# Optimization experiments

Hardware: AMD Instinct MI355X
Metric: run time of the kernel (lower is better)

## Reference

```python
import jax, jax.numpy as jnp
import numpy as np

B, S, D, E = 32, 16, 64, 768  # batch, max summary segments, max doc splits, embed dim
EPS = 1e-12


def _l2norm(x):
    # tf.nn.l2_normalize: x * rsqrt(max(sum(x^2), eps))
    return x * jax.lax.rsqrt(jnp.maximum(jnp.sum(x * x, axis=-1, keepdims=True), EPS))


def setup_inputs() -> dict:
    key = jax.random.key(0)
    ks = jax.random.split(key, 12)
    nd = jax.random.randint(ks[0], (B,), 1, D + 1)
    ns = jax.random.randint(ks[1], (B,), 1, S + 1)
    doc = jax.random.normal(ks[2], (B, D, E), jnp.float32)
    seg = jax.random.normal(ks[3], (B, S, E), jnp.float32)
    # emulate RaggedTensor.to_tensor(): zero padding beyond ragged lengths
    doc = doc * (jnp.arange(D)[None, :, None] < nd[:, None, None])
    seg = seg * (jnp.arange(S)[None, :, None] < ns[:, None, None])
    tis = jax.random.uniform(ks[4], (B, S), jnp.float32)
    tis = jnp.where(jnp.arange(S)[None, :] < ns[:, None], tis, 1.0)
    tagg = jax.random.uniform(ks[5], (B,), jnp.float32)
    s1, s2, s3 = 1.0 / np.sqrt(2 * E), 1.0 / np.sqrt(E), 1.0 / np.sqrt(E // 2)
    W1 = jax.random.normal(ks[6], (2 * E, E), jnp.float32) * s1
    W2 = jax.random.normal(ks[7], (E, E // 2), jnp.float32) * s2
    W3 = jax.random.normal(ks[8], (E // 2, 1), jnp.float32) * s3
    return {
        'document_splits_embedding': doc,
        'summary_sentences_embedding': seg,
        'num_document_splits': nd,
        'num_summary_segments': ns,
        'target_agg_score': tagg,
        'target_instance_score': tis,
        'W1': W1, 'b1': jnp.zeros((E,), jnp.float32),
        'W2': W2, 'b2': jnp.zeros((E // 2,), jnp.float32),
        'W3': W3, 'b3': jnp.zeros((1,), jnp.float32),
    }


def reference(document_splits_embedding, summary_sentences_embedding,
              num_document_splits, num_summary_segments,
              target_agg_score, target_instance_score,
              W1, b1, W2, b2, W3, b3):
    doc, seg = document_splits_embedding, summary_sentences_embedding
    nd, ns = num_document_splits, num_summary_segments
    b, d, e = doc.shape
    s = seg.shape[1]
    nsf = ns.astype(jnp.float32)

    # target_instance_score padded with 1.0 beyond ragged length (done in setup; pass through)
    tis = target_instance_score

    # ---- pairwise MLP over all (segment, doc_split) pairs ----
    pair = jnp.concatenate([
        jnp.broadcast_to(doc[:, None, :, :], (b, s, d, e)),
        jnp.broadcast_to(seg[:, :, None, :], (b, s, d, e)),
    ], axis=-1)                                             # [B,S,D,2E]
    h = jax.nn.gelu(pair @ W1 + b1, approximate=False)      # [B,S,D,E]
    h = jax.nn.gelu(h @ W2 + b2, approximate=False)         # [B,S,D,E/2]
    mlp_out = jax.nn.sigmoid(h @ W3 + b3)[..., 0]           # [B,S,D]

    doc_mask = (jnp.arange(d)[None, :] < nd[:, None]).astype(jnp.float32)  # [B,D]
    scored = doc_mask[:, None, :] * mlp_out                # mask invalid doc splits
    pred0 = jnp.max(scored, axis=2)                         # [B,S]
    seg_scale = jnp.where(ns > 10, 1.0, 100.0)[:, None]     # faithful to mask+(1-mask)*100
    pred = seg_scale * pred0                                # [B,S]

    # ---- cosine similarity prior (keras CosineSimilarity = -cos) ----
    dn = _l2norm(doc)                                       # [B,D,E]
    sn = _l2norm(seg)                                       # [B,S,E]
    cos = jnp.einsum('bse,bde->bsd', sn, dn)                # [B,S,D]
    sim = doc_mask[:, None, :] * (1.0 + (-cos)) / 2.0
    doc_cos = jnp.max(sim, axis=2)                          # [B,S]
    seg_mask = (jnp.arange(s)[None, :] < ns[:, None]).astype(jnp.float32)
    diff = jnp.abs(doc_cos - pred) * seg_mask
    cos_prior = jnp.mean(jnp.sum(diff, axis=1) / nsf)

    # ---- correlation prior: Pearson correlation over the 768 'sample' axis ----
    c = seg - jnp.mean(seg, axis=-1, keepdims=True)
    z = c * jax.lax.rsqrt(jnp.maximum(jnp.sum(c * c, axis=-1, keepdims=True), EPS))
    R = (1.0 + jnp.einsum('bse,bte->bst', z, z)) / 2.0      # [B,S,S]
    p = pred
    t1 = (1.0 - p)[:, :, None] * (1.0 - p)[:, None, :]
    t2 = p[:, :, None] * p[:, None, :]
    pair_mask = seg_mask[:, :, None] * seg_mask[:, None, :]
    term = jnp.abs(t1 - R) * jnp.abs(t2 - R) * pair_mask
    corr_prior = jnp.mean(jnp.sum(term, axis=(1, 2)) / nsf)

    return (target_agg_score, tis, pred, ns, cos_prior, corr_prior)
```

## Files before the change

### kernel.cpp

```cpp
#include <hip/hip_runtime.h>
#include <hip/hip_bf16.h>
#include <math.h>

#define EPSF 1e-12f

typedef short bf16x8 __attribute__((ext_vector_type(8)));
typedef float f32x4  __attribute__((ext_vector_type(4)));

__device__ __forceinline__ float gelu_fast(float x) {
    float x2 = x * x;
    float z = -2.3021184f * x * fmaf(0.044715f, x2, 1.0f);
    float u = __builtin_amdgcn_exp2f(z);
    return x * __builtin_amdgcn_rcpf(1.0f + u);
}
__device__ __forceinline__ float sigmoid_fast(float x) {
    float u = __builtin_amdgcn_exp2f(-1.44269504f * x);
    return __builtin_amdgcn_rcpf(1.0f + u);
}
__device__ __forceinline__ float bf2f(unsigned short u) {
    return __uint_as_float(((unsigned int)u) << 16);
}
__device__ __forceinline__ unsigned short f2bf(float f) {
    unsigned int u = __float_as_uint(f);
    u += 0x7FFFu + ((u >> 16) & 1u);
    return (unsigned short)(u >> 16);
}

__global__ __launch_bounds__(256) void k_prep(
    const float* __restrict__ doc, const float* __restrict__ seg,
    const float* __restrict__ W1, const float* __restrict__ W2,
    const float* __restrict__ tagg, const float* __restrict__ tis,
    const int* __restrict__ ns,
    float* __restrict__ dscale, float* __restrict__ sscale,
    float* __restrict__ smean, float* __restrict__ cscale,
    unsigned short* __restrict__ docB, unsigned short* __restrict__ segB,
    unsigned short* __restrict__ W1T, unsigned short* __restrict__ W2T,
    float* __restrict__ out)
{
    __shared__ float sT[64][65];
    int blk = blockIdx.x;
    int t = threadIdx.x;
    if (blk == 1000) {
        if (t < 32) out[t] = tagg[t];
        out[32 + t] = tis[t];
        out[32 + 256 + t] = tis[256 + t];
        if (t < 32) out[1056 + t] = (float)ns[t];
        return;
    }
    if (blk < 640) {
        int row = blk * 4 + (t >> 6);
        int lane = t & 63;
        const float* src = (row < 2048) ? (doc + (size_t)row * 768)
                                        : (seg + (size_t)(row - 2048) * 768);
        unsigned short* dst = (row < 2048) ? (docB + (size_t)row * 768)
                                           : (segB + (size_t)(row - 2048) * 768);
        float ss = 0.f, sm = 0.f;
        float4 v0 = *(const float4*)(src + lane * 4);
        float4 v1 = *(const float4*)(src + lane * 4 + 256);
        float4 v2 = *(const float4*)(src + lane * 4 + 512);
        ss += v0.x * v0.x + v0.y * v0.y + v0.z * v0.z + v0.w * v0.w;
        ss += v1.x * v1.x + v1.y * v1.y + v1.z * v1.z + v1.w * v1.w;
        ss += v2.x * v2.x + v2.y * v2.y + v2.z * v2.z + v2.w * v2.w;
        sm += v0.x + v0.y + v0.z + v0.w;
        sm += v1.x + v1.y + v1.z + v1.w;
        sm += v2.x + v2.y + v2.z + v2.w;
        {
            ushort4 o;
            o.x = f2bf(v0.x); o.y = f2bf(v0.y); o.z = f2bf(v0.z); o.w = f2bf(v0.w);
            *(ushort4*)(dst + lane * 4) = o;
            o.x = f2bf(v1.x); o.y = f2bf(v1.y); o.z = f2bf(v1.z); o.w = f2bf(v1.w);
            *(ushort4*)(dst + lane * 4 + 256) = o;
            o.x = f2bf(v2.x); o.y = f2bf(v2.y); o.z = f2bf(v2.z); o.w = f2bf(v2.w);
            *(ushort4*)(dst + lane * 4 + 512) = o;
        }
        #pragma unroll
        for (int off = 32; off > 0; off >>= 1) {
            ss += __shfl_down(ss, off);
            sm += __shfl_down(sm, off);
        }
        if (lane == 0) {
            if (row < 2048) {
                dscale[row] = rsqrtf(fmaxf(ss, EPSF));
            } else {
                int r = row - 2048;
                sscale[r] = rsqrtf(fmaxf(ss, EPSF));
                float mean = sm * (1.0f / 768.0f);
                smean[r] = mean;
                cscale[r] = rsqrtf(fmaxf(ss - sm * mean, EPSF));
            }
        }
        return;
    }
    int tt = blk - 640;
    const float* in; unsigned short* out2; int R, C, bx, by;
    if (tt < 288) { in = W1; out2 = W1T; R = 1536; C = 768; bx = tt % 12; by = tt / 12; }
    else { tt -= 288; in = W2; out2 = W2T; R = 768; C = 384; bx = tt % 6; by = tt / 6; }
    int c0 = bx * 64, r0 = by * 64;
    int tr = t >> 2, tc4 = (t & 3) * 16;
    #pragma unroll
    for (int i = 0; i < 4; ++i) {
        float4 v = *(const float4*)(in + (size_t)(r0 + tr) * C + c0 + tc4 + i * 4);
        sT[tr][tc4 + i * 4 + 0] = v.x; sT[tr][tc4 + i * 4 + 1] = v.y;
        sT[tr][tc4 + i * 4 + 2] = v.z; sT[tr][tc4 + i * 4 + 3] = v.w;
    }
    __syncthreads();
    union { uint4 v; unsigned short u[8]; } o0, o1;
    #pragma unroll
    for (int i = 0; i < 8; ++i) o0.u[i] = f2bf(sT[tc4 + i][tr]);
    #pragma unroll
    for (int i = 0; i < 8; ++i) o1.u[i] = f2bf(sT[tc4 + 8 + i][tr]);
    *(uint4*)(out2 + (size_t)(c0 + tr) * R + r0 + tc4) = o0.v;
    *(uint4*)(out2 + (size_t)(c0 + tr) * R + r0 + tc4 + 8) = o1.v;
}

__global__ __launch_bounds__(256) void k_l1(
    const unsigned short* __restrict__ docB, const unsigned short* __restrict__ segB,
    const unsigned short* __restrict__ W1T_bf, const float* __restrict__ b1,
    unsigned short* __restrict__ XdocB, unsigned short* __restrict__ XsegB)
{
    int mb = blockIdx.x;
    int n0 = blockIdx.y * 128;
    int t = threadIdx.x, w = t >> 6, l = t & 63;
    int lm = l & 15, kh = l >> 4;
    bool isdoc = (mb < 32);
    int m0 = isdoc ? mb * 64 : (mb - 32) * 64;
    const unsigned short* A = isdoc ? docB : segB;
    int koff = isdoc ? 0 : 768;
    unsigned short* C = isdoc ? XdocB : XsegB;

    const unsigned short* gA = A + (size_t)(m0 + lm) * 768 + kh * 8;
    const unsigned short* gB = W1T_bf + (size_t)(n0 + w * 32 + lm) * 1536 + koff + kh * 8;

    f32x4 acc[4][2];
    #pragma unroll
    for (int mt = 0; mt < 4; ++mt)
        #pragma unroll
        for (int nt = 0; nt < 2; ++nt) acc[mt][nt] = (f32x4){0.f, 0.f, 0.f, 0.f};

    bf16x8 a0A[4], a1A[4], b0A[2], b1A[2];
    bf16x8 a0B[4], a1B[4], b0B[2], b1B[2];
    #pragma unroll
    for (int mt = 0; mt < 4; ++mt) {
        a0A[mt] = *(const bf16x8*)(gA + (size_t)mt * 16 * 768);
        a1A[mt] = *(const bf16x8*)(gA + (size_t)mt * 16 * 768 + 32);
    }
    #pragma unroll
    for (int nt = 0; nt < 2; ++nt) {
        b0A[nt] = *(const bf16x8*)(gB + (size_t)nt * 16 * 1536);
        b1A[nt] = *(const bf16x8*)(gB + (size_t)nt * 16 * 1536 + 32);
    }

    #define L1_BODY(KT, A0, A1, B0, B1, NA0, NA1, NB0, NB1)                     \
    {                                                                           \
        if ((KT) < 11) {                                                        \
            int ko = ((KT) + 1) * 64;                                           \
            _Pragma("unroll")                                                   \
            for (int mt = 0; mt < 4; ++mt) {                                    \
                NA0[mt] = *(const bf16x8*)(gA + (size_t)mt * 16 * 768 + ko);    \
                NA1[mt] = *(const bf16x8*)(gA + (size_t)mt * 16 * 768 + ko + 32); \
            }                                                                   \
            _Pragma("unroll")                                                   \
            for (int nt = 0; nt < 2; ++nt) {                                    \
                NB0[nt] = *(const bf16x8*)(gB + (size_t)nt * 16 * 1536 + ko);   \
                NB1[nt] = *(const bf16x8*)(gB + (size_t)nt * 16 * 1536 + ko + 32); \
            }                                                                   \
        }                                                                       \
        _Pragma("unroll")                                                       \
        for (int mt = 0; mt < 4; ++mt)                                          \
            _Pragma("unroll")                                                   \
            for (int nt = 0; nt < 2; ++nt)                                      \
                acc[mt][nt] = __builtin_amdgcn_mfma_f32_16x16x32_bf16(          \
                    A0[mt], B0[nt], acc[mt][nt], 0, 0, 0);                      \
        _Pragma("unroll")                                                       \
        for (int mt = 0; mt < 4; ++mt)                                          \
            _Pragma("unroll")                                                   \
            for (int nt = 0; nt < 2; ++nt)                                      \
                acc[mt][nt] = __builtin_amdgcn_mfma_f32_16x16x32_bf16(          \
                    A1[mt], B1[nt], acc[mt][nt], 0, 0, 0);                      \
    }

    for (int kt2 = 0; kt2 < 12; kt2 += 2) {
        L1_BODY(kt2,     a0A, a1A, b0A, b1A, a0B, a1B, b0B, b1B);
        L1_BODY(kt2 + 1, a0B, a1B, b0B, b1B, a0A, a1A, b0A, b1A);
    }
    #undef L1_BODY

    #pragma unroll
    for (int nt = 0; nt < 2; ++nt) {
        int n = n0 + w * 32 + nt * 16 + lm;
        float bv = isdoc ? 0.f : b1[n];
        #pragma unroll
        for (int mt = 0; mt < 4; ++mt)
            #pragma unroll
            for (int j = 0; j < 4; ++j) {
                int row = m0 + mt * 16 + kh * 4 + j;
                C[(size_t)row * 768 + n] = f2bf(acc[mt][nt][j] + bv);
            }
    }
}

__global__ __launch_bounds__(256, 2) void k_fused_mfma(
    const unsigned short* __restrict__ XdocB, const unsigned short* __restrict__ XsegB,
    const unsigned short* __restrict__ W2T_bf,
    const float* __restrict__ b2, const float* __restrict__ W3, const float* __restrict__ b3,
    const int* __restrict__ nd, const int* __restrict__ ns,
    const unsigned short* __restrict__ docB, const unsigned short* __restrict__ segB,
    const float* __restrict__ seg,
    const float* __restrict__ dscale, const float* __restrict__ sscale,
    const float* __restrict__ smean, const float* __restrict__ cscale,
    float* __restrict__ out_pred, float* __restrict__ predv,
    float* __restrict__ dcws, float* __restrict__ Rws)
{
    __shared__ union {
        struct {
            unsigned short sA0[64 * 64];
            unsigned short sA1[64 * 64];
            float sXseg[768];
            float sRed[64][4];
        } p;
        struct { float sRedC[16][4]; } c;
        struct { unsigned short zb[16][776]; } r;
    } U;

    int blk = blockIdx.x;
    int t = threadIdx.x, w = t >> 6, l = t & 63;
    int lm = l & 15, kh = l >> 4;

    if (blk >= 512) {
        if (blk < 544) {
            int b = blk - 512;
            const unsigned short* gS = segB + (size_t)(b * 16 + lm) * 768 + kh * 8;
            const unsigned short* gD = docB + (size_t)(b * 64 + w * 16 + lm) * 768 + kh * 8;
            f32x4 acc = (f32x4){0.f, 0.f, 0.f, 0.f};
            for (int kt = 0; kt < 24; ++kt) {
                bf16x8 a = *(const bf16x8*)(gS + kt * 32);
                bf16x8 bb = *(const bf16x8*)(gD + kt * 32);
                acc = __builtin_amdgcn_mfma_f32_16x16x32_bf16(a, bb, acc, 0, 0, 0);
            }
            int ndb = nd[b];
            int d = w * 16 + lm;
            float dsc = dscale[b * 64 + d];
            #pragma unroll
            for (int j = 0; j < 4; ++j) {
                int s = kh * 4 + j;
                float cosv = acc[j] * sscale[b * 16 + s] * dsc;
                float sim = (d < ndb) ? (1.0f - cosv) * 0.5f : 0.f;
                sim = fmaxf(sim, __shfl_xor(sim, 1));
                sim = fmaxf(sim, __shfl_xor(sim, 2));
                sim = fmaxf(sim, __shfl_xor(sim, 4));
                sim = fmaxf(sim, __shfl_xor(sim, 8));
                if (lm == 0) U.c.sRedC[s][w] = sim;
            }
            __syncthreads();
            if (t < 16) {
                float dc = fmaxf(fmaxf(U.c.sRedC[t][0], U.c.sRedC[t][1]),
                                 fmaxf(U.c.sRedC[t][2], U.c.sRedC[t][3]));
                dcws[b * 16 + t] = dc;
            }
        } else {
            int b = blk - 544;
            for (int i = t; i < 16 * 768; i += 256) {
                int s = i / 768; int e = i - s * 768;
                U.r.zb[s][e] = f2bf((seg[((size_t)b * 16 + s) * 768 + e]
                                     - smean[b * 16 + s]) * cscale[b * 16 + s]);
            }
            __syncthreads();
            if (w == 0) {
                f32x4 acc = (f32x4){0.f, 0.f, 0.f, 0.f};
                #pragma unroll
                for (int kt = 0; kt < 24; ++kt) {
                    bf16x8 z = *(const bf16x8*)&U.r.zb[lm][kt * 32 + kh * 8];
                    acc = __builtin_amdgcn_mfma_f32_16x16x32_bf16(z, z, acc, 0, 0, 0);
                }
                #pragma unroll
                for (int j = 0; j < 4; ++j) {
                    int row = kh * 4 + j;
                    Rws[b * 256 + row * 16 + lm] = 0.5f * (1.0f + acc[j]);
                }
            }
        }
        return;
    }

    int bs = ((blk & 7) << 6) | (blk >> 3);
    int b = bs >> 4;
    int sw2 = (lm & 7) << 4;

    for (int i = t; i < 768; i += 256) U.p.sXseg[i] = bf2f(XsegB[(size_t)bs * 768 + i]);

    const int ndb = nd[b];
    const float segscale = (ns[b] > 10) ? 1.0f : 100.0f;
    const float b3v = b3[0];

    f32x4 acc[4][6];
    #pragma unroll
    for (int mt = 0; mt < 4; ++mt)
        #pragma unroll
        for (int nt = 0; nt < 6; ++nt) acc[mt][nt] = (f32x4){0.f, 0.f, 0.f, 0.f};

    int ar = t >> 2, ak = (t & 3) * 16;
    int asw = (ar & 7) << 4;
    const char* gXd = (const char*)XdocB + (size_t)(b * 64 + ar) * 1536;
    const unsigned short* gW2w = W2T_bf + (size_t)(w * 96 + lm) * 768 + kh * 8;

    union u128 { uint4 v; unsigned short u[8]; };

    bf16x8 bbA[6], bbB[6];
    #pragma unroll
    for (int nt = 0; nt < 6; ++nt)
        bbA[nt] = *(const bf16x8*)(gW2w + (size_t)nt * 16 * 768);

    {
        u128 xc0, xc1;
        xc0.v = *(const uint4*)(gXd + ak * 2);
        xc1.v = *(const uint4*)(gXd + ak * 2 + 16);
        __syncthreads();
        u128 o0, o1;
        #pragma unroll
        for (int i = 0; i < 8; ++i)
            o0.u[i] = f2bf(gelu_fast(bf2f(xc0.u[i]) + U.p.sXseg[ak + i]));
        #pragma unroll
        for (int i = 0; i < 8; ++i)
            o1.u[i] = f2bf(gelu_fast(bf2f(xc1.u[i]) + U.p.sXseg[ak + 8 + i]));
        *(uint4*)((char*)U.p.sA0 + ar * 128 + ((ak * 2) ^ asw)) = o0.v;
        *(uint4*)((char*)U.p.sA0 + ar * 128 + ((ak * 2 + 16) ^ asw)) = o1.v;
    }

    #pragma unroll
    for (int kt = 0; kt < 12; ++kt) {
        unsigned short* cbuf = (kt & 1) ? U.p.sA1 : U.p.sA0;
        unsigned short* nbuf = (kt & 1) ? U.p.sA0 : U.p.sA1;
        __syncthreads();
        u128 xn0, xn1;
        if (kt < 11) {
            xn0.v = *(const uint4*)(gXd + (kt + 1) * 128 + ak * 2);
            xn1.v = *(const uint4*)(gXd + (kt + 1) * 128 + ak * 2 + 16);
        }
        {
            #pragma unroll
            for (int nt = 0; nt < 6; ++nt)
                bbB[nt] = *(const bf16x8*)(gW2w + (size_t)nt * 16 * 768 + kt * 64 + 32);
            int kb = (kh * 16) ^ sw2;
            bf16x8 a[4];
            #pragma unroll
            for (int mt = 0; mt < 4; ++mt)
                a[mt] = *(const bf16x8*)((const char*)cbuf + (mt * 16 + lm) * 128 + kb);
            __builtin_amdgcn_s_setprio(1);
            #pragma unroll
            for (int mt = 0; mt < 4; ++mt)
                #pragma unroll
                for (int nt = 0; nt < 6; ++nt)
                    acc[mt][nt] = __builtin_amdgcn_mfma_f32_16x16x32_bf16(
                        a[mt], bbA[nt], acc[mt][nt], 0, 0, 0);
            __builtin_amdgcn_s_setprio(0);
        }
        {
            if (kt < 11) {
                #pragma unroll
                for (int nt = 0; nt < 6; ++nt)
                    bbA[nt] = *(const bf16x8*)(gW2w + (size_t)nt * 16 * 768 + (kt + 1) * 64);
            }
            int kb = (64 + kh * 16) ^ sw2;
            bf16x8 a[4];
            #pragma unroll
            for (int mt = 0; mt < 4; ++mt)
                a[mt] = *(const bf16x8*)((const char*)cbuf + (mt * 16 + lm) * 128 + kb);
            __builtin_amdgcn_s_setprio(1);
            #pragma unroll
            for (int mt = 0; mt < 4; ++mt)
                #pragma unroll
                for (int nt = 0; nt < 6; ++nt)
                    acc[mt][nt] = __builtin_amdgcn_mfma_f32_16x16x32_bf16(
                        a[mt], bbB[nt], acc[mt][nt], 0, 0, 0);
            __builtin_amdgcn_s_setprio(0);
        }
        if (kt < 11) {
            u128 o0, o1;
            #pragma unroll
            for (int i = 0; i < 8; ++i)
                o0.u[i] = f2bf(gelu_fast(bf2f(xn0.u[i]) + U.p.sXseg[(kt + 1) * 64 + ak + i]));
            #pragma unroll
            for (int i = 0; i < 8; ++i)
                o1.u[i] = f2bf(gelu_fast(bf2f(xn1.u[i]) + U.p.sXseg[(kt + 1) * 64 + ak + 8 + i]));
            *(uint4*)((char*)nbuf + ar * 128 + ((ak * 2) ^ asw)) = o0.v;
            *(uint4*)((char*)nbuf + ar * 128 + ((ak * 2 + 16) ^ asw)) = o1.v;
        }
    }

    float b2v[6], w3v[6];
    #pragma unroll
    for (int nt = 0; nt < 6; ++nt) {
        int n = w * 96 + nt * 16 + lm;
        b2v[nt] = b2[n]; w3v[nt] = W3[n];
    }
    #pragma unroll
    for (int mt = 0; mt < 4; ++mt) {
        #pragma unroll
        for (int j = 0; j < 4; ++j) {
            float s = 0.f;
            #pragma unroll
            for (int nt = 0; nt < 6; ++nt)
                s += gelu_fast(acc[mt][nt][j] + b2v[nt]) * w3v[nt];
            s += __shfl_xor(s, 1); s += __shfl_xor(s, 2);
            s += __shfl_xor(s, 4); s += __shfl_xor(s, 8);
            if (lm == 0) U.p.sRed[mt * 16 + kh * 4 + j][w] = s;
        }
    }
    __syncthreads();
    if (w == 0) {
        float h3 = U.p.sRed[l][0] + U.p.sRed[l][1] + U.p.sRed[l][2] + U.p.sRed[l][3] + b3v;
        float sig = sigmoid_fast(h3);
        float val = (l < ndb) ? sig : 0.f;
        #pragma unroll
        for (int off = 32; off > 0; off >>= 1) val = fmaxf(val, __shfl_xor(val, off));
        if (l == 0) {
            float pv = segscale * val;
            out_pred[bs] = pv;
            predv[bs] = pv;
        }
    }
}

__global__ __launch_bounds__(256) void k_final(
    const int* __restrict__ ns, const float* __restrict__ dcws,
    const float* __restrict__ Rws, const float* __restrict__ predv,
    float* __restrict__ out)
{
    __shared__ float sl1[32], sl2[32];
    int t = threadIdx.x;
    if (t < 32) {
        int nsb = ns[t];
        float sb = 0.f;
        #pragma unroll
        for (int s = 0; s < 16; ++s) {
            float d = fabsf(dcws[t * 16 + s] - predv[t * 16 + s]);
            sb += (s < nsb) ? d : 0.f;
        }
        sl1[t] = sb / (float)nsb;
    }
    {
        int b = t >> 3, c = t & 7;
        int nsb = ns[b];
        float sum = 0.f;
        #pragma unroll
        for (int k = 0; k < 32; ++k) {
            int idx = c * 32 + k;
            int s = idx >> 4, tt = idx & 15;
            float R = Rws[b * 256 + idx];
            float ps = predv[b * 16 + s], pt = predv[b * 16 + tt];
            float t1 = (1.f - ps) * (1.f - pt), t2 = ps * pt;
            float term = fabsf(t1 - R) * fabsf(t2 - R);
            sum += (s < nsb && tt < nsb) ? term : 0.f;
        }
        sum += __shfl_xor(sum, 1);
        sum += __shfl_xor(sum, 2);
        sum += __shfl_xor(sum, 4);
        if (c == 0) sl2[b] = sum / (float)nsb;
    }
    __syncthreads();
    if (t == 0) {
        float a = 0.f, bsum = 0.f;
        #pragma unroll
        for (int i = 0; i < 32; ++i) { a += sl1[i]; bsum += sl2[i]; }
        out[1088] = a * (1.0f / 32.0f);
        out[1089] = bsum * (1.0f / 32.0f);
    }
}

extern "C" void kernel_launch(void* const* d_in, const int* in_sizes, int n_in,
                              void* d_out, int out_size, void* d_ws, size_t ws_size,
                              hipStream_t stream)
{
    const float* doc  = (const float*)d_in[0];
    const float* seg  = (const float*)d_in[1];
    const int*   nd   = (const int*)d_in[2];
    const int*   ns   = (const int*)d_in[3];
    const float* tagg = (const float*)d_in[4];
    const float* tis  = (const float*)d_in[5];
    const float* W1   = (const float*)d_in[6];
    const float* b1   = (const float*)d_in[7];
    const float* W2   = (const float*)d_in[8];
    const float* b2   = (const float*)d_in[9];
    const float* W3   = (const float*)d_in[10];
    const float* b3   = (const float*)d_in[11];
    float* out = (float*)d_out;

    float* fws      = (float*)d_ws;
    float* dscale   = fws;
    float* sscale   = dscale + 2048;
    float* smean    = sscale + 512;
    float* cscale   = smean + 512;
    float* predv    = cscale + 512;
    float* dcws     = predv + 512;
    float* Rws      = dcws + 512;
    unsigned short* docB  = (unsigned short*)(Rws + 8192);
    unsigned short* segB  = docB + (size_t)2048 * 768;
    unsigned short* W1T   = segB + (size_t)512 * 768;
    unsigned short* W2T   = W1T + (size_t)768 * 1536;
    unsigned short* XdocB = W2T + (size_t)384 * 768;
    unsigned short* XsegB = XdocB + (size_t)2048 * 768;

    k_prep<<<1001, 256, 0, stream>>>(doc, seg, W1, W2, tagg, tis, ns,
                                     dscale, sscale, smean, cscale,
                                     docB, segB, W1T, W2T, out);
    k_l1<<<dim3(40, 6), 256, 0, stream>>>(docB, segB, W1T, b1, XdocB, XsegB);
    k_fused_mfma<<<576, 256, 0, stream>>>(XdocB, XsegB, W2T, b2, W3, b3, nd, ns,
                                          docB, segB, seg, dscale, sscale,
                                          smean, cscale, out + 544, predv,
                                          dcws, Rws);
    k_final<<<1, 256, 0, stream>>>(ns, dcws, Rws, predv, out);
}
```

Before: 82.78 us.

## Process two summary segments per block with 512 threads sharing W2 fragments

The fused layer-2 kernel now handles two summary segments per block, using 8 waves that each own 48 output columns. The doc-side load is reused to build gelu activations for both segments, and each W2 fragment feeds MFMAs for both. The grid shrinks from 576 to 320 blocks of 512 threads. This cuts redundant XdocB and W2 traffic per segment, at the cost of more LDS, fewer blocks (256 compute blocks on many CUs) and half-idle waves in the cos and correlation side blocks.

```diff
diff --git a/kernel.cpp b/kernel.cpp
--- a/kernel.cpp
+++ b/kernel.cpp
@@ -199,7 +199,7 @@
     }
 }
 
-__global__ __launch_bounds__(256, 2) void k_fused_mfma(
+__global__ __launch_bounds__(512, 2) void k_fused_mfma(
     const unsigned short* __restrict__ XdocB, const unsigned short* __restrict__ XsegB,
     const unsigned short* __restrict__ W2T_bf,
     const float* __restrict__ b2, const float* __restrict__ W3, const float* __restrict__ b3,
@@ -213,10 +213,9 @@
 {
     __shared__ union {
         struct {
-            unsigned short sA0[64 * 64];
-            unsigned short sA1[64 * 64];
-            float sXseg[768];
-            float sRed[64][4];
+            unsigned short sA[2][2][64 * 64];
+            float sXseg[2][768];
+            float sRed[2][64][8];
         } p;
         struct { float sRedC[16][4]; } c;
         struct { unsigned short zb[16][776]; } r;
@@ -225,31 +224,34 @@
     int blk = blockIdx.x;
     int t = threadIdx.x, w = t >> 6, l = t & 63;
     int lm = l & 15, kh = l >> 4;
-
-    if (blk >= 512) {
-        if (blk < 544) {
-            int b = blk - 512;
-            const unsigned short* gS = segB + (size_t)(b * 16 + lm) * 768 + kh * 8;
-            const unsigned short* gD = docB + (size_t)(b * 64 + w * 16 + lm) * 768 + kh * 8;
-            f32x4 acc = (f32x4){0.f, 0.f, 0.f, 0.f};
-            for (int kt = 0; kt < 24; ++kt) {
-                bf16x8 a = *(const bf16x8*)(gS + kt * 32);
-                bf16x8 bb = *(const bf16x8*)(gD + kt * 32);
-                acc = __builtin_amdgcn_mfma_f32_16x16x32_bf16(a, bb, acc, 0, 0, 0);
-            }
-            int ndb = nd[b];
-            int d = w * 16 + lm;
-            float dsc = dscale[b * 64 + d];
-            #pragma unroll
-            for (int j = 0; j < 4; ++j) {
-                int s = kh * 4 + j;
-                float cosv = acc[j] * sscale[b * 16 + s] * dsc;
-                float sim = (d < ndb) ? (1.0f - cosv) * 0.5f : 0.f;
-                sim = fmaxf(sim, __shfl_xor(sim, 1));
-                sim = fmaxf(sim, __shfl_xor(sim, 2));
-                sim = fmaxf(sim, __shfl_xor(sim, 4));
-                sim = fmaxf(sim, __shfl_xor(sim, 8));
-                if (lm == 0) U.c.sRedC[s][w] = sim;
+    union u128 { uint4 v; unsigned short u[8]; };
+
+    if (blk >= 256) {
+        if (blk < 288) {
+            int b = blk - 256;
+            if (w < 4) {
+                const unsigned short* gS = segB + (size_t)(b * 16 + lm) * 768 + kh * 8;
+                const unsigned short* gD = docB + (size_t)(b * 64 + w * 16 + lm) * 768 + kh * 8;
+                f32x4 acc = (f32x4){0.f, 0.f, 0.f, 0.f};
+                for (int kt = 0; kt < 24; ++kt) {
+                    bf16x8 a = *(const bf16x8*)(gS + kt * 32);
+                    bf16x8 bb = *(const bf16x8*)(gD + kt * 32);
+                    acc = __builtin_amdgcn_mfma_f32_16x16x32_bf16(a, bb, acc, 0, 0, 0);
+                }
+                int ndb = nd[b];
+                int d = w * 16 + lm;
+                float dsc = dscale[b * 64 + d];
+                #pragma unroll
+                for (int j = 0; j < 4; ++j) {
+                    int s = kh * 4 + j;
+                    float cosv = acc[j] * sscale[b * 16 + s] * dsc;
+                    float sim = (d < ndb) ? (1.0f - cosv) * 0.5f : 0.f;
+                    sim = fmaxf(sim, __shfl_xor(sim, 1));
+                    sim = fmaxf(sim, __shfl_xor(sim, 2));
+                    sim = fmaxf(sim, __shfl_xor(sim, 4));
+                    sim = fmaxf(sim, __shfl_xor(sim, 8));
+                    if (lm == 0) U.c.sRedC[s][w] = sim;
+                }
             }
             __syncthreads();
             if (t < 16) {
@@ -258,8 +260,8 @@
                 dcws[b * 16 + t] = dc;
             }
         } else {
-            int b = blk - 544;
-            for (int i = t; i < 16 * 768; i += 256) {
+            int b = blk - 288;
+            for (int i = t; i < 16 * 768; i += 512) {
                 int s = i / 768; int e = i - s * 768;
                 U.r.zb[s][e] = f2bf((seg[((size_t)b * 16 + s) * 768 + e]
                                      - smean[b * 16 + s]) * cscale[b * 16 + s]);
@@ -282,141 +284,158 @@
         return;
     }
 
-    int bs = ((blk & 7) << 6) | (blk >> 3);
-    int b = bs >> 4;
+    int b = blk & 31;
+    int spair = blk >> 5;
+    int bs0 = b * 16 + spair * 2;
     int sw2 = (lm & 7) << 4;
 
-    for (int i = t; i < 768; i += 256) U.p.sXseg[i] = bf2f(XsegB[(size_t)bs * 768 + i]);
+    for (int i = t; i < 1536; i += 512) {
+        int ss = i >> 9 >= 0 ? (i / 768) : 0;
+        int e = i - ss * 768;
+        U.p.sXseg[ss][e] = bf2f(XsegB[(size_t)(bs0 + ss) * 768 + e]);
+    }
 
     const int ndb = nd[b];
     const float segscale = (ns[b] > 10) ? 1.0f : 100.0f;
     const float b3v = b3[0];
 
-    f32x4 acc[4][6];
+    f32x4 acc[4][3][2];
     #pragma unroll
     for (int mt = 0; mt < 4; ++mt)
         #pragma unroll
-        for (int nt = 0; nt < 6; ++nt) acc[mt][nt] = (f32x4){0.f, 0.f, 0.f, 0.f};
-
-    int ar = t >> 2, ak = (t & 3) * 16;
+        for (int nt = 0; nt < 3; ++nt)
+            #pragma unroll
+            for (int ss = 0; ss < 2; ++ss)
+                acc[mt][nt][ss] = (f32x4){0.f, 0.f, 0.f, 0.f};
+
+    int ar = t >> 3, ci = t & 7;
     int asw = (ar & 7) << 4;
     const char* gXd = (const char*)XdocB + (size_t)(b * 64 + ar) * 1536;
-    const unsigned short* gW2w = W2T_bf + (size_t)(w * 96 + lm) * 768 + kh * 8;
-
-    union u128 { uint4 v; unsigned short u[8]; };
+    const unsigned short* gW2w = W2T_bf + (size_t)(w * 48 + lm) * 768 + kh * 8;
 
     bf16x8 bbA[6], bbB[6];
     #pragma unroll
-    for (int nt = 0; nt < 6; ++nt)
-        bbA[nt] = *(const bf16x8*)(gW2w + (size_t)nt * 16 * 768);
+    for (int j = 0; j < 6; ++j)
+        bbA[j] = *(const bf16x8*)(gW2w + (size_t)(j % 3) * 16 * 768 + (j / 3) * 32);
 
     {
-        u128 xc0, xc1;
-        xc0.v = *(const uint4*)(gXd + ak * 2);
-        xc1.v = *(const uint4*)(gXd + ak * 2 + 16);
+        u128 xc;
+        xc.v = *(const uint4*)(gXd + ci * 16);
         __syncthreads();
         u128 o0, o1;
         #pragma unroll
-        for (int i = 0; i < 8; ++i)
-            o0.u[i] = f2bf(gelu_fast(bf2f(xc0.u[i]) + U.p.sXseg[ak + i]));
-        #pragma unroll
-        for (int i = 0; i < 8; ++i)
-            o1.u[i] = f2bf(gelu_fast(bf2f(xc1.u[i]) + U.p.sXseg[ak + 8 + i]));
-        *(uint4*)((char*)U.p.sA0 + ar * 128 + ((ak * 2) ^ asw)) = o0.v;
-        *(uint4*)((char*)U.p.sA0 + ar * 128 + ((ak * 2 + 16) ^ asw)) = o1.v;
+        for (int i = 0; i < 8; ++i) {
+            float xd = bf2f(xc.u[i]);
+            o0.u[i] = f2bf(gelu_fast(xd + U.p.sXseg[0][ci * 8 + i]));
+            o1.u[i] = f2bf(gelu_fast(xd + U.p.sXseg[1][ci * 8 + i]));
+        }
+        *(uint4*)((char*)U.p.sA[0][0] + ar * 128 + ((ci * 16) ^ asw)) = o0.v;
+        *(uint4*)((char*)U.p.sA[1][0] + ar * 128 + ((ci * 16) ^ asw)) = o1.v;
     }
 
     #pragma unroll
     for (int kt = 0; kt < 12; ++kt) {
-        unsigned short* cbuf = (kt & 1) ? U.p.sA1 : U.p.sA0;
-        unsigned short* nbuf = (kt & 1) ? U.p.sA0 : U.p.sA1;
+        int cb = kt & 1, nb = cb ^ 1;
         __syncthreads();
-        u128 xn0, xn1;
-        if (kt < 11) {
-            xn0.v = *(const uint4*)(gXd + (kt + 1) * 128 + ak * 2);
-            xn1.v = *(const uint4*)(gXd + (kt + 1) * 128 + ak * 2 + 16);
-        }
+        u128 xn;
+        if (kt < 11) xn.v = *(const uint4*)(gXd + (kt + 1) * 128 + ci * 16);
         {
             #pragma unroll
-            for (int nt = 0; nt < 6; ++nt)
-                bbB[nt] = *(const bf16x8*)(gW2w + (size_t)nt * 16 * 768 + kt * 64 + 32);
+            for (int j = 0; j < 3; ++j)
+                bbB[3 + j] = *(const bf16x8*)(gW2w + (size_t)j * 16 * 768 + kt * 64 + 32);
             int kb = (kh * 16) ^ sw2;
-            bf16x8 a[4];
+            bf16x8 a0[4], a1[4];
+            #pragma unroll
+            for (int mt = 0; mt < 4; ++mt) {
+                a0[mt] = *(const bf16x8*)((const char*)U.p.sA[0][cb] + (mt * 16 + lm) * 128 + kb);
+                a1[mt] = *(const bf16x8*)((const char*)U.p.sA[1][cb] + (mt * 16 + lm) * 128 + kb);
+            }
+            __builtin_amdgcn_s_setprio(1);
             #pragma unroll
             for (int mt = 0; mt < 4; ++mt)
-                a[mt] = *(const bf16x8*)((const char*)cbuf + (mt * 16 + lm) * 128 + kb);
-            __builtin_amdgcn_s_setprio(1);
-            #pragma unroll
-            for (int mt = 0; mt < 4; ++mt)
-                #pragma unroll
-                for (int nt = 0; nt < 6; ++nt)
-                    acc[mt][nt] = __builtin_amdgcn_mfma_f32_16x16x32_bf16(
-                        a[mt], bbA[nt], acc[mt][nt], 0, 0, 0);
+                #pragma unroll
+                for (int nt = 0; nt < 3; ++nt) {
+                    acc[mt][nt][0] = __builtin_amdgcn_mfma_f32_16x16x32_bf16(
+                        a0[mt], bbA[nt], acc[mt][nt][0], 0, 0, 0);
+                    acc[mt][nt][1] = __builtin_amdgcn_mfma_f32_16x16x32_bf16(
+                        a1[mt], bbA[nt], acc[mt][nt][1], 0, 0, 0);
+                }
             __builtin_amdgcn_s_setprio(0);
         }
         {
             if (kt < 11) {
                 #pragma unroll
-                for (int nt = 0; nt < 6; ++nt)
-                    bbA[nt] = *(const bf16x8*)(gW2w + (size_t)nt * 16 * 768 + (kt + 1) * 64);
+                for (int j = 0; j < 3; ++j)
+                    bbA[j] = *(const bf16x8*)(gW2w + (size_t)j * 16 * 768 + (kt + 1) * 64);
             }
             int kb = (64 + kh * 16) ^ sw2;
-            bf16x8 a[4];
+            bf16x8 a0[4], a1[4];
+            #pragma unroll
+            for (int mt = 0; mt < 4; ++mt) {
+                a0[mt] = *(const bf16x8*)((const char*)U.p.sA[0][cb] + (mt * 16 + lm) * 128 + kb);
+                a1[mt] = *(const bf16x8*)((const char*)U.p.sA[1][cb] + (mt * 16 + lm) * 128 + kb);
+            }
+            __builtin_amdgcn_s_setprio(1);
             #pragma unroll
             for (int mt = 0; mt < 4; ++mt)
-                a[mt] = *(const bf16x8*)((const char*)cbuf + (mt * 16 + lm) * 128 + kb);
-            __builtin_amdgcn_s_setprio(1);
-            #pragma unroll
-            for (int mt = 0; mt < 4; ++mt)
-                #pragma unroll
-                for (int nt = 0; nt < 6; ++nt)
-                    acc[mt][nt] = __builtin_amdgcn_mfma_f32_16x16x32_bf16(
-                        a[mt], bbB[nt], acc[mt][nt], 0, 0, 0);
+                #pragma unroll
+                for (int nt = 0; nt < 3; ++nt) {
+                    acc[mt][nt][0] = __builtin_amdgcn_mfma_f32_16x16x32_bf16(
+                        a0[mt], bbB[3 + nt], acc[mt][nt][0], 0, 0, 0);
+                    acc[mt][nt][1] = __builtin_amdgcn_mfma_f32_16x16x32_bf16(
+                        a1[mt], bbB[3 + nt], acc[mt][nt][1], 0, 0, 0);
+                }
             __builtin_amdgcn_s_setprio(0);
         }
         if (kt < 11) {
             u128 o0, o1;
             #pragma unroll
-            for (int i = 0; i < 8; ++i)
-                o0.u[i] = f2bf(gelu_fast(bf2f(xn0.u[i]) + U.p.sXseg[(kt + 1) * 64 + ak + i]));
-            #pragma unroll
-            for (int i = 0; i < 8; ++i)
-                o1.u[i] = f2bf(gelu_fast(bf2f(xn1.u[i]) + U.p.sXseg[(kt + 1) * 64 + ak + 8 + i]));
-            *(uint4*)((char*)nbuf + ar * 128 + ((ak * 2) ^ asw)) = o0.v;
-            *(uint4*)((char*)nbuf + ar * 128 + ((ak * 2 + 16) ^ asw)) = o1.v;
-        }
-    }
-
-    float b2v[6], w3v[6];
-    #pragma unroll
-    for (int nt = 0; nt < 6; ++nt) {
-        int n = w * 96 + nt * 16 + lm;
+            for (int i = 0; i < 8; ++i) {
+                float xd = bf2f(xn.u[i]);
+                o0.u[i] = f2bf(gelu_fast(xd + U.p.sXseg[0][(kt + 1) * 64 + ci * 8 + i]));
+                o1.u[i] = f2bf(gelu_fast(xd + U.p.sXseg[1][(kt + 1) * 64 + ci * 8 + i]));
+            }
+            *(uint4*)((char*)U.p.sA[0][nb] + ar * 128 + ((ci * 16) ^ asw)) = o0.v;
+            *(uint4*)((char*)U.p.sA[1][nb] + ar * 128 + ((ci * 16) ^ asw)) = o1.v;
+        }
+    }
+
+    float b2v[3], w3v[3];
+    #pragma unroll
+    for (int nt = 0; nt < 3; ++nt) {
+        int n = w * 48 + nt * 16 + lm;
         b2v[nt] = b2[n]; w3v[nt] = W3[n];
     }
     #pragma unroll
-    for (int mt = 0; mt < 4; ++mt) {
-        #pragma unroll
-        for (int j = 0; j < 4; ++j) {
-            float s = 0.f;
-            #pragma unroll
-            for (int nt = 0; nt < 6; ++nt)
-                s += gelu_fast(acc[mt][nt][j] + b2v[nt]) * w3v[nt];
-            s += __shfl_xor(s, 1); s += __shfl_xor(s, 2);
-            s += __shfl_xor(s, 4); s += __shfl_xor(s, 8);
-            if (lm == 0) U.p.sRed[mt * 16 + kh * 4 + j][w] = s;
+    for (int ss = 0; ss < 2; ++ss) {
+        #pragma unroll
+        for (int mt = 0; mt < 4; ++mt) {
+            #pragma unroll
+            for (int j = 0; j < 4; ++j) {
+                float s = 0.f;
+                #pragma unroll
+                for (int nt = 0; nt < 3; ++nt)
+                    s += gelu_fast(acc[mt][nt][ss][j] + b2v[nt]) * w3v[nt];
+                s += __shfl_xor(s, 1); s += __shfl_xor(s, 2);
+                s += __shfl_xor(s, 4); s += __shfl_xor(s, 8);
+                if (lm == 0) U.p.sRed[ss][mt * 16 + kh * 4 + j][w] = s;
+            }
         }
     }
     __syncthreads();
-    if (w == 0) {
-        float h3 = U.p.sRed[l][0] + U.p.sRed[l][1] + U.p.sRed[l][2] + U.p.sRed[l][3] + b3v;
+    if (w < 2) {
+        int ss = w;
+        float h3 = b3v;
+        #pragma unroll
+        for (int j = 0; j < 8; ++j) h3 += U.p.sRed[ss][l][j];
         float sig = sigmoid_fast(h3);
         float val = (l < ndb) ? sig : 0.f;
         #pragma unroll
         for (int off = 32; off > 0; off >>= 1) val = fmaxf(val, __shfl_xor(val, off));
         if (l == 0) {
             float pv = segscale * val;
-            out_pred[bs] = pv;
-            predv[bs] = pv;
+            out_pred[bs0 + ss] = pv;
+            predv[bs0 + ss] = pv;
         }
     }
 }
@@ -504,7 +523,7 @@
                                      dscale, sscale, smean, cscale,
                                      docB, segB, W1T, W2T, out);
     k_l1<<<dim3(40, 6), 256, 0, stream>>>(docB, segB, W1T, b1, XdocB, XsegB);
-    k_fused_mfma<<<576, 256, 0, stream>>>(XdocB, XsegB, W2T, b2, W3, b3, nd, ns,
+    k_fused_mfma<<<320, 512, 0, stream>>>(XdocB, XsegB, W2T, b2, W3, b3, nd, ns,
                                           docB, segB, seg, dscale, sscale,
                                           smean, cscale, out + 544, predv,
                                           dcws, Rws);
```

Result: slower. 87.83 us (+6.1%).
